# Kernel optimization log

Measured on AMD Instinct MI355X. Metric: run time of the kernel, lower is better.

The kernel has to match this reference:

```python
import jax, jax.numpy as jnp
import numpy as np

EMBED_DIM = 1024
NUM_HEADS = 16
PROJ_DIM = EMBED_DIM // NUM_HEADS


def setup_inputs() -> dict:
    key = jax.random.key(0)
    ks = jax.random.split(key, 11)
    B, S, D = 2, 2048, EMBED_DIM
    scale = 1.0 / np.sqrt(D)
    inp = {
        'q': jax.random.normal(ks[0], (B, S, D), jnp.float32),
        'k': jax.random.normal(ks[1], (B, S, D), jnp.float32),
        'v': jax.random.normal(ks[2], (B, S, D), jnp.float32),
        'Wq': jax.random.normal(ks[3], (D, D), jnp.float32) * scale,
        'bq': jnp.zeros((D,), jnp.float32),
        'Wk': jax.random.normal(ks[4], (D, D), jnp.float32) * scale,
        'bk': jnp.zeros((D,), jnp.float32),
        'Wv': jax.random.normal(ks[5], (D, D), jnp.float32) * scale,
        'bv': jnp.zeros((D,), jnp.float32),
        'Wo': jax.random.normal(ks[6], (D, D), jnp.float32) * scale,
        'bo': jnp.zeros((D,), jnp.float32),
        'use_causal_mask': 1,
    }
    return inp


def _split_heads(x, B):
    # [B, S, D] -> [B, H, S, Pd]
    return x.reshape(B, -1, NUM_HEADS, PROJ_DIM).transpose(0, 2, 1, 3)


def reference(q, k, v, Wq, bq, Wk, bk, Wv, bv, Wo, bo, use_causal_mask):
    B, S, D = q.shape
    qh = _split_heads(q @ Wq + bq, B)
    kh = _split_heads(k @ Wk + bk, B)
    vh = _split_heads(v @ Wv + bv, B)
    # scaled dot-product attention; scores [B, H, S, S]
    logits = jnp.einsum('bhqd,bhkd->bhqk', qh, kh) / jnp.sqrt(
        jnp.asarray(PROJ_DIM, jnp.float32))
    if use_causal_mask:
        # faithful to source: logits += log(tril * 1e-9 + 1e-9)
        tril = jnp.tril(jnp.ones((S, S), dtype=logits.dtype))
        logits = logits + jnp.log(tril * 1e-9 + 1e-9)
    attn = jax.nn.softmax(logits, axis=-1)
    out = jnp.einsum('bhqk,bhkd->bhqd', attn, vh)
    out = out.transpose(0, 2, 1, 3).reshape(B, S, D)
    return out @ Wo + bo
```

## Files before the change

kernel.cpp:

```cpp
#include <hip/hip_runtime.h>
#include <hip/hip_bf16.h>
#include <stdint.h>

#define EMBED 1024
#define NH    16
#define PD    64
#define BATCH 2
#define SEQ   2048

typedef unsigned short u16;
typedef __attribute__((ext_vector_type(8))) short bf16x8;
typedef __attribute__((ext_vector_type(4))) float f32x4;

#define WAITALL() __builtin_amdgcn_s_waitcnt(0)

__device__ __forceinline__ float b2f(u16 x) {
  unsigned u = ((unsigned)x) << 16;
  return __builtin_bit_cast(float, u);
}
__device__ __forceinline__ u16 cvtb(float x) {
  __bf16 h = (__bf16)x;
  return __builtin_bit_cast(u16, h);
}
__device__ __forceinline__ float loadIn(const void* p, size_t i, int isf32) {
  return isf32 ? ((const float*)p)[i] : b2f(((const u16*)p)[i]);
}
__device__ __forceinline__ void async16(const void* g, void* l) {
  __builtin_amdgcn_global_load_lds((const __attribute__((address_space(1))) void*)g,
                                   (__attribute__((address_space(3))) void*)l,
                                   16, 0, 0);
}
__device__ __forceinline__ int detect_f32(const void* q) {
  unsigned w0 = ((const unsigned*)q)[threadIdx.x & 63];
  unsigned e = (w0 >> 7) & 0xffu;
  unsigned long long m = __ballot(e >= 110 && e <= 135);
  return (__popcll(m) < 32) ? 1 : 0;
}

__global__ __launch_bounds__(256) void conv_fused(
    const void* q, const void* k, const void* v,
    const void* Wq, const void* Wk, const void* Wv, const void* Wo,
    u16* qb, u16* kb, u16* vb, u16* WT_all) {
  __shared__ float sh[64][65];
  const int isf32 = detect_f32(q);

  if (blockIdx.y < 3) {
    size_t i = ((size_t)blockIdx.x * 256 + threadIdx.x) * 8;
    const void* src = (blockIdx.y == 0) ? q : (blockIdx.y == 1) ? k : v;
    u16* dst = (blockIdx.y == 0) ? qb : (blockIdx.y == 1) ? kb : vb;
    u16 tmp[8];
    if (isf32) {
      const float* s = (const float*)src + i;
      float4 a = *(const float4*)s;
      float4 b = *(const float4*)(s + 4);
      tmp[0] = cvtb(a.x); tmp[1] = cvtb(a.y); tmp[2] = cvtb(a.z); tmp[3] = cvtb(a.w);
      tmp[4] = cvtb(b.x); tmp[5] = cvtb(b.y); tmp[6] = cvtb(b.z); tmp[7] = cvtb(b.w);
    } else {
      const uint4 r = *(const uint4*)((const u16*)src + i);
      *(uint4*)tmp = r;
    }
    *(uint4*)(dst + i) = *(uint4*)tmp;
    return;
  }

  if (blockIdx.x >= 1024) return;
  const int z = blockIdx.x >> 8;
  const int xy = blockIdx.x & 255;
  const int bx = xy & 15, by = xy >> 4;
  const void* W = (z == 0) ? Wq : (z == 1) ? Wk : (z == 2) ? Wv : Wo;
  u16* WT = WT_all + (size_t)z * EMBED * EMBED;
  int r0 = by * 64, c0 = bx * 64;
  int col = threadIdx.x & 63;
  int rb  = threadIdx.x >> 6;
#pragma unroll
  for (int i = 0; i < 16; i++) {
    int row = i * 4 + rb;
    sh[row][col] = loadIn(W, (size_t)(r0 + row) * EMBED + c0 + col, isf32);
  }
  __syncthreads();
#pragma unroll
  for (int i = 0; i < 16; i++) {
    int row = i * 4 + rb;
    WT[(size_t)(c0 + row) * EMBED + r0 + col] = cvtb(sh[col][row]);
  }
}

__device__ __forceinline__ void gemm_stage(const u16* __restrict__ A,
                                           const u16* __restrict__ Bt,
                                           int tm, int tn, int kt,
                                           u16* As, u16* Bs, int tid) {
#pragma unroll
  for (int i = 0; i < 4; i++) {
    int c = i * 256 + tid;
    int row = c >> 3;
    int col = ((c & 7) << 3) ^ ((row & 7) << 3);
    async16(A + (size_t)(tm + row) * EMBED + kt + col, As + c * 8);
    async16(Bt + (size_t)(tn + row) * EMBED + kt + col, Bs + c * 8);
  }
}

__device__ __forceinline__ void gemm_compute(const u16* As, const u16* Bs,
                                             int wm, int wn, int l15, int quad,
                                             int rbx, f32x4 acc[4][4]) {
#pragma unroll
  for (int ks = 0; ks < 64; ks += 32) {
    int ko = (ks + quad * 8) ^ rbx;
    bf16x8 af[4], bf[4];
#pragma unroll
    for (int mt = 0; mt < 4; mt++)
      af[mt] = *(const bf16x8*)(As + (wm + mt * 16 + l15) * 64 + ko);
#pragma unroll
    for (int nt = 0; nt < 4; nt++)
      bf[nt] = *(const bf16x8*)(Bs + (wn + nt * 16 + l15) * 64 + ko);
#pragma unroll
    for (int mt = 0; mt < 4; mt++)
#pragma unroll
      for (int nt = 0; nt < 4; nt++)
        acc[mt][nt] = __builtin_amdgcn_mfma_f32_16x16x32_bf16(
            af[mt], bf[nt], acc[mt][nt], 0, 0, 0);
  }
}

__global__ __launch_bounds__(256) void qkv_gemm(
    const u16* qb, const u16* kb, const u16* vb, const u16* wts,
    const void* bq, const void* bk, const void* bv,
    u16* Qh, u16* Kh, u16* Vt, const void* qorig) {
  __shared__ __align__(16) u16 lds[4 * 128 * 64];
  const int isf32 = detect_f32(qorig);
  int z = blockIdx.z;
  const u16* A = (z == 0) ? qb : (z == 1) ? kb : vb;
  const u16* Bt = wts + (size_t)z * EMBED * EMBED;
  const void* bias = (z == 0) ? bq : (z == 1) ? bk : bv;
  int tm = blockIdx.y * 128, tn = blockIdx.x * 128;

  const int tid = threadIdx.x, lane = tid & 63, wv = tid >> 6;
  const int wm = (wv >> 1) * 64, wn = (wv & 1) * 64;
  const int l15 = lane & 15, quad = lane >> 4;
  const int rbx = (lane & 7) << 3;
  f32x4 acc[4][4];
  f32x4 zz = {0.f, 0.f, 0.f, 0.f};
#pragma unroll
  for (int i = 0; i < 4; i++)
#pragma unroll
    for (int j = 0; j < 4; j++) acc[i][j] = zz;

  gemm_stage(A, Bt, tm, tn, 0, lds, lds + 8192, tid);
  WAITALL();
  __syncthreads();
  for (int kt = 0; kt < EMBED; kt += 64) {
    const int cur = (kt >> 6) & 1;
    u16* curb = lds + cur * 16384;
    if (kt + 64 < EMBED)
      gemm_stage(A, Bt, tm, tn, kt + 64, lds + (cur ^ 1) * 16384,
                 lds + (cur ^ 1) * 16384 + 8192, tid);
    gemm_compute(curb, curb + 8192, wm, wn, l15, quad, rbx, acc);
    WAITALL();
    __syncthreads();
  }

  int rbase = tm + wm + (quad << 2);
  int cbase = tn + wn + l15;
  if (z < 2) {
    u16* dst = (z == 0) ? Qh : Kh;
#pragma unroll
    for (int mt = 0; mt < 4; mt++)
#pragma unroll
      for (int nt = 0; nt < 4; nt++) {
        int col = cbase + nt * 16;
        float bv_ = loadIn(bias, col, isf32);
        int h = col >> 6, p = col & 63;
#pragma unroll
        for (int j = 0; j < 4; j++) {
          int row = rbase + mt * 16 + j;
          int b = row >> 11, s = row & 2047;
          dst[(((size_t)(b * NH + h) * SEQ) + s) * PD + p] =
              cvtb(acc[mt][nt][j] + bv_);
        }
      }
  } else {
#pragma unroll
    for (int mt = 0; mt < 4; mt++)
#pragma unroll
      for (int nt = 0; nt < 4; nt++) {
        int col = cbase + nt * 16;
        float bv_ = loadIn(bias, col, isf32);
        int h = col >> 6, p = col & 63;
        int row0 = rbase + mt * 16;
        int b = row0 >> 11, s0 = row0 & 2047;
        int beta = s0 >> 5, w = s0 & 31;
        int pos = (beta << 5) + (((w >> 2) & 3) << 3) + ((w >> 4) << 2);
        ushort4 pk;
        pk.x = cvtb(acc[mt][nt][0] + bv_);
        pk.y = cvtb(acc[mt][nt][1] + bv_);
        pk.z = cvtb(acc[mt][nt][2] + bv_);
        pk.w = cvtb(acc[mt][nt][3] + bv_);
        *(ushort4*)(Vt + ((size_t)(b * NH + h) * PD + p) * SEQ + pos) = pk;
      }
  }
}

__global__ __launch_bounds__(256, 4) void attn(const u16* __restrict__ Qh,
                                               const u16* __restrict__ Kh,
                                               const u16* __restrict__ Vt,
                                               u16* __restrict__ O,
                                               const int* __restrict__ maskflag) {
  __shared__ __align__(16) u16 sh[4 * 64 * 64];
  u16* const Ksb0 = sh;
  u16* const Ksb1 = sh + 4096;
  u16* const Vsb0 = sh + 8192;
  u16* const Vsb1 = sh + 12288;
  u16* const Qs   = Ksb1;

  const int lid = blockIdx.x + (blockIdx.y << 5);
  const int xcd = lid & 7, j = lid >> 3;
  const int bh = (xcd << 2) | (j & 3);
  const int qt = (j >> 2) * 64;

  const int tid = threadIdx.x, lane = tid & 63, wv = tid >> 6;
  const int qh = wv & 1;
  const int kh = wv >> 1;
  const int l15 = lane & 15, quad = lane >> 4;
  const int rbx = (lane & 7) << 3;
  const size_t head = (size_t)bh * SEQ * PD;
  const bool causal = (maskflag[0] != 0);
  const float C = 0.18033688011112042f;

  const int c0 = tid, c1 = 256 + tid;
  const int r0 = c0 >> 3, r1 = c1 >> 3;
  const int x0 = ((c0 & 7) << 3) ^ ((r0 & 7) << 3);
  const int x1 = ((c1 & 7) << 3) ^ ((r1 & 7) << 3);

  async16(Qh + head + (size_t)(qt + r0) * PD + x0, Qs + c0 * 8);
  async16(Qh + head + (size_t)(qt + r1) * PD + x1, Qs + c1 * 8);
  async16(Kh + head + (size_t)r0 * PD + x0, Ksb0 + c0 * 8);
  async16(Kh + head + (size_t)r1 * PD + x1, Ksb0 + c1 * 8);
  async16(Vt + head + (size_t)r0 * SEQ + x0, Vsb0 + c0 * 8);
  async16(Vt + head + (size_t)r1 * SEQ + x1, Vsb0 + c1 * 8);
  WAITALL();
  __syncthreads();

  bf16x8 qf[2][2];
#pragma unroll
  for (int ks = 0; ks < 2; ks++) {
    int ko = (ks * 32 + quad * 8) ^ rbx;
    qf[ks][0] = *(const bf16x8*)(Qs + (qh * 32 + l15) * 64 + ko);
    qf[ks][1] = *(const bf16x8*)(Qs + (qh * 32 + 16 + l15) * 64 + ko);
  }
  __syncthreads();

  float lacc[2] = {0.f, 0.f};
  f32x4 oacc[4][2];
  f32x4 z4 = {0.f, 0.f, 0.f, 0.f};
#pragma unroll
  for (int mt = 0; mt < 4; mt++)
#pragma unroll
    for (int qx = 0; qx < 2; qx++) oacc[mt][qx] = z4;

  const int qrow0 = qt + qh * 32 + l15;

  for (int t = 0; t < SEQ / 64; t++) {
    const int k0 = t * 64;
    const int cur = t & 1;
    if (t + 1 < SEQ / 64) {
      const int kn = k0 + 64;
      u16* Kn = cur ? Ksb0 : Ksb1;
      u16* Vn = cur ? Vsb0 : Vsb1;
      async16(Kh + head + (size_t)(kn + r0) * PD + x0, Kn + c0 * 8);
      async16(Kh + head + (size_t)(kn + r1) * PD + x1, Kn + c1 * 8);
      async16(Vt + head + (size_t)r0 * SEQ + kn + x0, Vn + c0 * 8);
      async16(Vt + head + (size_t)r1 * SEQ + kn + x1, Vn + c1 * 8);
    }
    const u16* Ksc = cur ? Ksb1 : Ksb0;
    const u16* Vsc = cur ? Vsb1 : Vsb0;

    f32x4 st[2][2];
#pragma unroll
    for (int kx = 0; kx < 2; kx++)
#pragma unroll
      for (int qx = 0; qx < 2; qx++) st[kx][qx] = z4;
    __builtin_amdgcn_s_setprio(1);
#pragma unroll
    for (int ks = 0; ks < 2; ks++) {
      int ko = (ks * 32 + quad * 8) ^ rbx;
#pragma unroll
      for (int kx = 0; kx < 2; kx++) {
        bf16x8 kf = *(const bf16x8*)(Ksc + (kh * 32 + kx * 16 + l15) * 64 + ko);
        st[kx][0] = __builtin_amdgcn_mfma_f32_16x16x32_bf16(kf, qf[ks][0], st[kx][0], 0, 0, 0);
        st[kx][1] = __builtin_amdgcn_mfma_f32_16x16x32_bf16(kf, qf[ks][1], st[kx][1], 0, 0, 0);
      }
    }
    __builtin_amdgcn_s_setprio(0);

    const int mode = !causal ? 0 : (k0 > qt + 63 ? 2 : (k0 + 63 <= qt ? 0 : 1));
    const float ub = (mode == 2) ? -17.f : -16.f;
    unsigned pw[2][4];
#pragma unroll
    for (int kx = 0; kx < 2; kx++) {
#pragma unroll
      for (int qx = 0; qx < 2; qx++) {
        const int qrow = qrow0 + qx * 16;
        float p[4];
#pragma unroll
        for (int r = 0; r < 4; r++) {
          float bias = ub;
          if (mode == 1) {
            int kappa = k0 + kh * 32 + kx * 16 + 4 * quad + r;
            bias = (kappa > qrow) ? -17.f : -16.f;
          }
          p[r] = exp2f(fmaf(st[kx][qx][r], C, bias));
        }
        lacc[qx] += (p[0] + p[1]) + (p[2] + p[3]);
        pw[qx][kx * 2 + 0] =
            (unsigned)cvtb(p[0]) | ((unsigned)cvtb(p[1]) << 16);
        pw[qx][kx * 2 + 1] =
            (unsigned)cvtb(p[2]) | ((unsigned)cvtb(p[3]) << 16);
      }
    }

    __builtin_amdgcn_s_setprio(1);
    bf16x8 pf0 = __builtin_bit_cast(bf16x8,
        (uint4){pw[0][0], pw[0][1], pw[0][2], pw[0][3]});
    bf16x8 pf1 = __builtin_bit_cast(bf16x8,
        (uint4){pw[1][0], pw[1][1], pw[1][2], pw[1][3]});
#pragma unroll
    for (int mt = 0; mt < 4; mt++) {
      int row = mt * 16 + l15;
      int chunk = ((kh << 2) + quad) ^ (row & 7);
      bf16x8 vf = *(const bf16x8*)(Vsc + row * 64 + (chunk << 3));
      oacc[mt][0] = __builtin_amdgcn_mfma_f32_16x16x32_bf16(vf, pf0, oacc[mt][0], 0, 0, 0);
      oacc[mt][1] = __builtin_amdgcn_mfma_f32_16x16x32_bf16(vf, pf1, oacc[mt][1], 0, 0, 0);
    }
    __builtin_amdgcn_s_setprio(0);
    WAITALL();
    __syncthreads();
  }

#pragma unroll
  for (int qx = 0; qx < 2; qx++) {
    lacc[qx] += __shfl_xor(lacc[qx], 16, 64);
    lacc[qx] += __shfl_xor(lacc[qx], 32, 64);
  }

  float* red = (float*)sh;
  if (kh == 1) {
#pragma unroll
    for (int mt = 0; mt < 4; mt++)
#pragma unroll
      for (int qx = 0; qx < 2; qx++)
        *(f32x4*)(red + qh * 2048 + (mt * 2 + qx) * 256 + lane * 4) =
            oacc[mt][qx];
    red[4096 + qh * 128 + lane] = lacc[0];
    red[4096 + qh * 128 + 64 + lane] = lacc[1];
  }
  __syncthreads();
  if (kh == 0) {
    float l0 = lacc[0] + red[4096 + qh * 128 + lane];
    float l1 = lacc[1] + red[4096 + qh * 128 + 64 + lane];
    float inv[2] = {1.f / l0, 1.f / l1};
    const int b = bh >> 4, h = bh & 15;
#pragma unroll
    for (int mt = 0; mt < 4; mt++) {
#pragma unroll
      for (int qx = 0; qx < 2; qx++) {
        f32x4 o = oacc[mt][qx] +
                  *(const f32x4*)(red + qh * 2048 + (mt * 2 + qx) * 256 + lane * 4);
        int qrow = qrow0 + qx * 16;
        ushort4 w;
        w.x = cvtb(o[0] * inv[qx]);
        w.y = cvtb(o[1] * inv[qx]);
        w.z = cvtb(o[2] * inv[qx]);
        w.w = cvtb(o[3] * inv[qx]);
        *(ushort4*)(O + ((size_t)b * SEQ + qrow) * EMBED + h * PD + mt * 16 +
                    4 * quad) = w;
      }
    }
  }
}

__global__ __launch_bounds__(256) void out_gemm(const u16* __restrict__ Ob,
                                                const u16* __restrict__ WoT,
                                                const void* __restrict__ bo,
                                                void* __restrict__ out,
                                                const void* __restrict__ qorig) {
  __shared__ __align__(16) u16 lds[4 * 128 * 64];
  const int isf32 = detect_f32(qorig);
  int tm = blockIdx.y * 128, tn = blockIdx.x * 128;
  const int tid = threadIdx.x, lane = tid & 63, wv = tid >> 6;
  const int wm = (wv >> 1) * 64, wn = (wv & 1) * 64;
  const int l15 = lane & 15, quad = lane >> 4;
  const int rbx = (lane & 7) << 3;
  f32x4 acc[4][4];
  f32x4 zz = {0.f, 0.f, 0.f, 0.f};
#pragma unroll
  for (int i = 0; i < 4; i++)
#pragma unroll
    for (int j = 0; j < 4; j++) acc[i][j] = zz;

  gemm_stage(Ob, WoT, tm, tn, 0, lds, lds + 8192, tid);
  WAITALL();
  __syncthreads();
  for (int kt = 0; kt < EMBED; kt += 64) {
    const int cur = (kt >> 6) & 1;
    u16* curb = lds + cur * 16384;
    if (kt + 64 < EMBED)
      gemm_stage(Ob, WoT, tm, tn, kt + 64, lds + (cur ^ 1) * 16384,
                 lds + (cur ^ 1) * 16384 + 8192, tid);
    gemm_compute(curb, curb + 8192, wm, wn, l15, quad, rbx, acc);
    WAITALL();
    __syncthreads();
  }

  int rbase = tm + wm + (quad << 2);
  int cbase = tn + wn + l15;
#pragma unroll
  for (int mt = 0; mt < 4; mt++)
#pragma unroll
    for (int nt = 0; nt < 4; nt++) {
      int col = cbase + nt * 16;
      float bv_ = loadIn(bo, col, isf32);
#pragma unroll
      for (int j = 0; j < 4; j++) {
        int row = rbase + mt * 16 + j;
        float val = acc[mt][nt][j] + bv_;
        size_t off = (size_t)row * EMBED + col;
        if (isf32) ((float*)out)[off] = val;
        else       ((u16*)out)[off]   = cvtb(val);
      }
    }
}

extern "C" void kernel_launch(void* const* d_in, const int* in_sizes, int n_in,
                              void* d_out, int out_size, void* d_ws, size_t ws_size,
                              hipStream_t stream) {
  const void* q  = d_in[0];
  const void* k  = d_in[1];
  const void* v  = d_in[2];
  const void* Wq = d_in[3];
  const void* bq = d_in[4];
  const void* Wk = d_in[5];
  const void* bk = d_in[6];
  const void* Wv = d_in[7];
  const void* bv = d_in[8];
  const void* Wo = d_in[9];
  const void* bo = d_in[10];
  const int* msk = (const int*)d_in[11];

  char* ws = (char*)d_ws;
  u16*  qb    = (u16*)(ws + 64);
  u16*  kb    = qb + (size_t)4194304;
  u16*  vb    = kb + (size_t)4194304;
  u16*  WT    = vb + (size_t)4194304;
  u16*  Qh    = WT + (size_t)4194304;
  u16*  Kh    = Qh + (size_t)4194304;
  u16*  Vt    = Kh + (size_t)4194304;
  u16*  Ob    = Vt + (size_t)4194304;

  conv_fused<<<dim3(2048, 4), 256, 0, stream>>>(q, k, v, Wq, Wk, Wv, Wo,
                                                qb, kb, vb, WT);
  qkv_gemm<<<dim3(8, 32, 3), 256, 0, stream>>>(qb, kb, vb, WT, bq, bk, bv,
                                               Qh, Kh, Vt, q);
  attn<<<dim3(32, 32), 256, 0, stream>>>(Qh, Kh, Vt, Ob, msk);
  out_gemm<<<dim3(8, 32), 256, 0, stream>>>(Ob, WT + (size_t)3 * 1048576,
                                            bo, d_out, q);
}
```

Measured before the change: 275.4 us.

## Triple-buffer K tiles and issue loads after a single top-of-loop barrier

Restructures the attention main loop so that K tiles are triple-buffered (prefetched two tiles ahead) and V tiles stay double-buffered. The full wait-all plus barrier at the end of each iteration is replaced by a partial vmcnt wait and one barrier at the top, so later loads can stay in flight while the current tile is computed. Shared memory grows from four to five 64x64 tiles, which may limit how many blocks fit per CU. The kernel now depends on exact vmcnt ordering and on the barrier before the Q-fragment read to guarantee that the initial async loads have landed.

```diff
diff --git a/kernel.cpp b/kernel.cpp
--- a/kernel.cpp
+++ b/kernel.cpp
@@ -204,12 +204,9 @@
                                                const u16* __restrict__ Vt,
                                                u16* __restrict__ O,
                                                const int* __restrict__ maskflag) {
-  __shared__ __align__(16) u16 sh[4 * 64 * 64];
-  u16* const Ksb0 = sh;
-  u16* const Ksb1 = sh + 4096;
-  u16* const Vsb0 = sh + 8192;
-  u16* const Vsb1 = sh + 12288;
-  u16* const Qs   = Ksb1;
+  __shared__ __align__(16) u16 sh[5 * 64 * 64];
+  u16* const Vbase = sh + 3 * 4096;
+  u16* const Qs    = sh + 2 * 4096;
 
   const int lid = blockIdx.x + (blockIdx.y << 5);
   const int xcd = lid & 7, j = lid >> 3;
@@ -232,11 +229,12 @@
 
   async16(Qh + head + (size_t)(qt + r0) * PD + x0, Qs + c0 * 8);
   async16(Qh + head + (size_t)(qt + r1) * PD + x1, Qs + c1 * 8);
-  async16(Kh + head + (size_t)r0 * PD + x0, Ksb0 + c0 * 8);
-  async16(Kh + head + (size_t)r1 * PD + x1, Ksb0 + c1 * 8);
-  async16(Vt + head + (size_t)r0 * SEQ + x0, Vsb0 + c0 * 8);
-  async16(Vt + head + (size_t)r1 * SEQ + x1, Vsb0 + c1 * 8);
-  WAITALL();
+  async16(Kh + head + (size_t)r0 * PD + x0, sh + c0 * 8);
+  async16(Kh + head + (size_t)r1 * PD + x1, sh + c1 * 8);
+  async16(Vt + head + (size_t)r0 * SEQ + x0, Vbase + c0 * 8);
+  async16(Vt + head + (size_t)r1 * SEQ + x1, Vbase + c1 * 8);
+  async16(Kh + head + (size_t)(64 + r0) * PD + x0, sh + 4096 + c0 * 8);
+  async16(Kh + head + (size_t)(64 + r1) * PD + x1, sh + 4096 + c1 * 8);
   __syncthreads();
 
   bf16x8 qf[2][2];
@@ -258,20 +256,32 @@
 
   const int qrow0 = qt + qh * 32 + l15;
 
+  int b0 = 0, b1 = 1, b2 = 2;
+
   for (int t = 0; t < SEQ / 64; t++) {
+    if (t == SEQ / 64 - 1) {
+      asm volatile("s_waitcnt vmcnt(0)" ::: "memory");
+    } else {
+      asm volatile("s_waitcnt vmcnt(2)" ::: "memory");
+    }
+    __builtin_amdgcn_sched_barrier(0);
+    __builtin_amdgcn_s_barrier();
+
     const int k0 = t * 64;
-    const int cur = t & 1;
     if (t + 1 < SEQ / 64) {
       const int kn = k0 + 64;
-      u16* Kn = cur ? Ksb0 : Ksb1;
-      u16* Vn = cur ? Vsb0 : Vsb1;
+      u16* Vn = Vbase + ((t + 1) & 1) * 4096;
+      async16(Vt + head + (size_t)r0 * SEQ + kn + x0, Vn + c0 * 8);
+      async16(Vt + head + (size_t)r1 * SEQ + kn + x1, Vn + c1 * 8);
+    }
+    if (t + 2 < SEQ / 64) {
+      const int kn = k0 + 128;
+      u16* Kn = sh + b2 * 4096;
       async16(Kh + head + (size_t)(kn + r0) * PD + x0, Kn + c0 * 8);
       async16(Kh + head + (size_t)(kn + r1) * PD + x1, Kn + c1 * 8);
-      async16(Vt + head + (size_t)r0 * SEQ + kn + x0, Vn + c0 * 8);
-      async16(Vt + head + (size_t)r1 * SEQ + kn + x1, Vn + c1 * 8);
-    }
-    const u16* Ksc = cur ? Ksb1 : Ksb0;
-    const u16* Vsc = cur ? Vsb1 : Vsb0;
+    }
+    const u16* Ksc = sh + b0 * 4096;
+    const u16* Vsc = Vbase + (t & 1) * 4096;
 
     f32x4 st[2][2];
 #pragma unroll
@@ -331,9 +341,11 @@
       oacc[mt][1] = __builtin_amdgcn_mfma_f32_16x16x32_bf16(vf, pf1, oacc[mt][1], 0, 0, 0);
     }
     __builtin_amdgcn_s_setprio(0);
-    WAITALL();
-    __syncthreads();
-  }
+
+    int tmp = b0; b0 = b1; b1 = b2; b2 = tmp;
+  }
+
+  __syncthreads();
 
 #pragma unroll
   for (int qx = 0; qx < 2; qx++) {
```

New measurement: 272.0 us. Within noise of the previous version (-1.2%).

## Load attention K/V fragments directly from global memory, dropping LDS staging

Applied to the files above, without the earlier changes.

The attention kernel no longer stages Q, K and V tiles through double-buffered shared memory with async copies and per-iteration barriers. Each wave now reads its own MFMA operand fragments straight from global memory into registers, and shared memory is kept only for the final cross-wave reduction. This removes the LDS round trip and the __syncthreads per key tile. In exchange, the two query-half waves fetch the same K/V data twice through the cache, and there is no explicit prefetch of the next tile to hide global-load latency.

```diff
diff --git a/kernel.cpp b/kernel.cpp
--- a/kernel.cpp
+++ b/kernel.cpp
@@ -204,12 +204,7 @@
                                                const u16* __restrict__ Vt,
                                                u16* __restrict__ O,
                                                const int* __restrict__ maskflag) {
-  __shared__ __align__(16) u16 sh[4 * 64 * 64];
-  u16* const Ksb0 = sh;
-  u16* const Ksb1 = sh + 4096;
-  u16* const Vsb0 = sh + 8192;
-  u16* const Vsb1 = sh + 12288;
-  u16* const Qs   = Ksb1;
+  __shared__ float red[4352];
 
   const int lid = blockIdx.x + (blockIdx.y << 5);
   const int xcd = lid & 7, j = lid >> 3;
@@ -220,33 +215,20 @@
   const int qh = wv & 1;
   const int kh = wv >> 1;
   const int l15 = lane & 15, quad = lane >> 4;
-  const int rbx = (lane & 7) << 3;
   const size_t head = (size_t)bh * SEQ * PD;
   const bool causal = (maskflag[0] != 0);
   const float C = 0.18033688011112042f;
 
-  const int c0 = tid, c1 = 256 + tid;
-  const int r0 = c0 >> 3, r1 = c1 >> 3;
-  const int x0 = ((c0 & 7) << 3) ^ ((r0 & 7) << 3);
-  const int x1 = ((c1 & 7) << 3) ^ ((r1 & 7) << 3);
-
-  async16(Qh + head + (size_t)(qt + r0) * PD + x0, Qs + c0 * 8);
-  async16(Qh + head + (size_t)(qt + r1) * PD + x1, Qs + c1 * 8);
-  async16(Kh + head + (size_t)r0 * PD + x0, Ksb0 + c0 * 8);
-  async16(Kh + head + (size_t)r1 * PD + x1, Ksb0 + c1 * 8);
-  async16(Vt + head + (size_t)r0 * SEQ + x0, Vsb0 + c0 * 8);
-  async16(Vt + head + (size_t)r1 * SEQ + x1, Vsb0 + c1 * 8);
-  WAITALL();
-  __syncthreads();
+  const u16* Kw = Kh + head + (size_t)(kh * 32 + l15) * PD + quad * 8;
+  const u16* Vw = Vt + head + (size_t)l15 * SEQ + (kh * 4 + quad) * 8;
+  const u16* Qw = Qh + head + (size_t)(qt + qh * 32 + l15) * PD + quad * 8;
 
   bf16x8 qf[2][2];
 #pragma unroll
   for (int ks = 0; ks < 2; ks++) {
-    int ko = (ks * 32 + quad * 8) ^ rbx;
-    qf[ks][0] = *(const bf16x8*)(Qs + (qh * 32 + l15) * 64 + ko);
-    qf[ks][1] = *(const bf16x8*)(Qs + (qh * 32 + 16 + l15) * 64 + ko);
-  }
-  __syncthreads();
+    qf[ks][0] = *(const bf16x8*)(Qw + ks * 32);
+    qf[ks][1] = *(const bf16x8*)(Qw + 16 * PD + ks * 32);
+  }
 
   float lacc[2] = {0.f, 0.f};
   f32x4 oacc[4][2];
@@ -260,18 +242,13 @@
 
   for (int t = 0; t < SEQ / 64; t++) {
     const int k0 = t * 64;
-    const int cur = t & 1;
-    if (t + 1 < SEQ / 64) {
-      const int kn = k0 + 64;
-      u16* Kn = cur ? Ksb0 : Ksb1;
-      u16* Vn = cur ? Vsb0 : Vsb1;
-      async16(Kh + head + (size_t)(kn + r0) * PD + x0, Kn + c0 * 8);
-      async16(Kh + head + (size_t)(kn + r1) * PD + x1, Kn + c1 * 8);
-      async16(Vt + head + (size_t)r0 * SEQ + kn + x0, Vn + c0 * 8);
-      async16(Vt + head + (size_t)r1 * SEQ + kn + x1, Vn + c1 * 8);
-    }
-    const u16* Ksc = cur ? Ksb1 : Ksb0;
-    const u16* Vsc = cur ? Vsb1 : Vsb0;
+
+    bf16x8 kf[2][2];
+#pragma unroll
+    for (int ks = 0; ks < 2; ks++)
+#pragma unroll
+      for (int kx = 0; kx < 2; kx++)
+        kf[ks][kx] = *(const bf16x8*)(Kw + (k0 + kx * 16) * PD + ks * 32);
 
     f32x4 st[2][2];
 #pragma unroll
@@ -280,16 +257,18 @@
       for (int qx = 0; qx < 2; qx++) st[kx][qx] = z4;
     __builtin_amdgcn_s_setprio(1);
 #pragma unroll
-    for (int ks = 0; ks < 2; ks++) {
-      int ko = (ks * 32 + quad * 8) ^ rbx;
+    for (int ks = 0; ks < 2; ks++)
 #pragma unroll
       for (int kx = 0; kx < 2; kx++) {
-        bf16x8 kf = *(const bf16x8*)(Ksc + (kh * 32 + kx * 16 + l15) * 64 + ko);
-        st[kx][0] = __builtin_amdgcn_mfma_f32_16x16x32_bf16(kf, qf[ks][0], st[kx][0], 0, 0, 0);
-        st[kx][1] = __builtin_amdgcn_mfma_f32_16x16x32_bf16(kf, qf[ks][1], st[kx][1], 0, 0, 0);
-      }
-    }
+        st[kx][0] = __builtin_amdgcn_mfma_f32_16x16x32_bf16(kf[ks][kx], qf[ks][0], st[kx][0], 0, 0, 0);
+        st[kx][1] = __builtin_amdgcn_mfma_f32_16x16x32_bf16(kf[ks][kx], qf[ks][1], st[kx][1], 0, 0, 0);
+      }
     __builtin_amdgcn_s_setprio(0);
+
+    bf16x8 vf[4];
+#pragma unroll
+    for (int mt = 0; mt < 4; mt++)
+      vf[mt] = *(const bf16x8*)(Vw + mt * 16 * SEQ + k0);
 
     const int mode = !causal ? 0 : (k0 > qt + 63 ? 2 : (k0 + 63 <= qt ? 0 : 1));
     const float ub = (mode == 2) ? -17.f : -16.f;
@@ -324,15 +303,10 @@
         (uint4){pw[1][0], pw[1][1], pw[1][2], pw[1][3]});
 #pragma unroll
     for (int mt = 0; mt < 4; mt++) {
-      int row = mt * 16 + l15;
-      int chunk = ((kh << 2) + quad) ^ (row & 7);
-      bf16x8 vf = *(const bf16x8*)(Vsc + row * 64 + (chunk << 3));
-      oacc[mt][0] = __builtin_amdgcn_mfma_f32_16x16x32_bf16(vf, pf0, oacc[mt][0], 0, 0, 0);
-      oacc[mt][1] = __builtin_amdgcn_mfma_f32_16x16x32_bf16(vf, pf1, oacc[mt][1], 0, 0, 0);
+      oacc[mt][0] = __builtin_amdgcn_mfma_f32_16x16x32_bf16(vf[mt], pf0, oacc[mt][0], 0, 0, 0);
+      oacc[mt][1] = __builtin_amdgcn_mfma_f32_16x16x32_bf16(vf[mt], pf1, oacc[mt][1], 0, 0, 0);
     }
     __builtin_amdgcn_s_setprio(0);
-    WAITALL();
-    __syncthreads();
   }
 
 #pragma unroll
@@ -341,7 +315,6 @@
     lacc[qx] += __shfl_xor(lacc[qx], 32, 64);
   }
 
-  float* red = (float*)sh;
   if (kh == 1) {
 #pragma unroll
     for (int mt = 0; mt < 4; mt++)
```

Measured after the change: 319.7 us. +16.1%, slower.
